# Performance work log

Hardware: AMD Instinct MI355X
Metric: run time of the kernel (lower is better)

Reference implementation:

```python
import jax, jax.numpy as jnp
import numpy as np

# dims: batch, seq, d_model, d_hidden, routed experts, top-k, shared experts
B, S, D, H, E_R, K, E_S = 2, 1024, 1024, 512, 64, 6, 2
EPS = 1.1920929e-07  # torch.finfo(float32).eps, RMSNorm default when eps=None


def setup_inputs() -> dict:
    key = jax.random.key(0)
    ks = jax.random.split(key, 8)
    u = lambda k, shape, b: jax.random.uniform(k, shape, jnp.float32, -b, b)
    bd = 1.0 / np.sqrt(D)   # bound for W1 (1/sqrt(d_input)) and W2 (1/sqrt(d_output)=1/sqrt(D))
    bh = 1.0 / np.sqrt(H)
    return {
        "x": jax.random.normal(ks[0], (B, S, D), jnp.float32),
        "norm_w": jnp.ones((D,), jnp.float32),            # RMSNorm weight
        "Wr": u(ks[1], (E_R, D), bd),                      # router Linear weight (no bias)
        "sW1": u(ks[2], (E_S, D, H), bd), "sb1": jnp.zeros((E_S, 1, H), jnp.float32),
        "sW2": u(ks[3], (E_S, H, D), bd), "sb2": jnp.zeros((E_S, 1, D), jnp.float32),
        "sWg": u(ks[4], (H, H), bh),                       # shared-experts SwiGLU gate weight
        "rW1": u(ks[5], (E_R, D, H), bd), "rb1": jnp.zeros((E_R, 1, H), jnp.float32),
        "rW2": u(ks[6], (E_R, H, D), bd), "rb2": jnp.zeros((E_R, 1, D), jnp.float32),
        "rWg": u(ks[7], (H, H), bh),                       # routed-experts SwiGLU gate weight
        "bias": jnp.full((E_R,), 1.0 / E_R, jnp.float32), # routing bias buffer (expert_bias=True)
    }


def _rmsnorm(x, w):
    ms = jnp.mean(x * x, axis=-1, keepdims=True)
    return x * jax.lax.rsqrt(ms + EPS) * w


def _swiglu(h, Wg):
    # SwiGLU(d_model=H): silu(h @ Wg) * h, elementwise gate over hidden dim
    return jax.nn.silu(h @ Wg) * h


def reference(x, norm_w, Wr, sW1, sb1, sW2, sb2, sWg, rW1, rb1, rW2, rb2, rWg, bias):
    xn = _rmsnorm(x, norm_w)
    t = xn.reshape(-1, D)                                  # (T, D) tokens
    # --- shared experts, summed over expert axis ---
    hs = jnp.einsum('td,edh->teh', t, sW1) + sb1[None, :, 0, :]
    hs = _swiglu(hs, sWg)
    shared = jnp.einsum('teh,ehd->td', hs, sW2) + jnp.sum(sb2[:, 0, :], axis=0)
    # --- router ---
    raw = t @ Wr.T                                         # (T, E_R) raw affinity
    aff = jax.lax.stop_gradient(raw) + bias                # detached + bias for top-k selection
    _, idx = jax.lax.top_k(aff, K)                         # (T, K)
    # --- routed experts: dense all-expert FFN, gather top-k outputs ---
    # (mathematically identical to the source's per-token weight gather,
    #  but avoids materializing (T,K,D,H) weight tensors)
    h = jnp.einsum('td,edh->teh', t, rW1) + rb1[None, :, 0, :]   # (T, E_R, H)
    h = _swiglu(h, rWg)
    out_all = jnp.einsum('teh,ehd->ted', h, rW2) + rb2[None, :, 0, :]  # (T, E_R, D)
    out_k = jnp.take_along_axis(out_all, idx[:, :, None], axis=1)      # (T, K, D)
    aff_k = jnp.take_along_axis(raw, idx, axis=1)                      # (T, K) raw (undetached)
    w = aff_k / jnp.sum(aff_k, axis=-1, keepdims=True)                 # expert_bias=True path
    routed = jnp.einsum('tk,tkd->td', w, out_k)                        # (T, D)
    return x + (shared + routed).reshape(B, S, D)
```

## Files before the change

### kernel.cpp

```cpp
#include <hip/hip_runtime.h>
#include <cstdint>
#include <cstddef>

typedef unsigned short u16;
typedef unsigned int u32;
typedef __attribute__((ext_vector_type(8))) short bh8;
typedef __attribute__((ext_vector_type(4))) float fx4;

#define T_TOK 2048
#define D_DIM 1024
#define H_DIM 512
#define N_EXP 64
#define K_TOP 6
#define N_ASG (T_TOK * K_TOP)

__device__ __forceinline__ float bf2f(u16 v) {
    union { u32 u; float f; } c; c.u = ((u32)v) << 16; return c.f;
}
__device__ __forceinline__ u16 f2bf(float f) {
    union { u32 u; float f; } c; c.f = f;
    u32 u = c.u;
    return (u16)((u + 0x7fffu + ((u >> 16) & 1u)) >> 16);
}

__global__ __launch_bounds__(256) void rmsnorm_k(
    const float* __restrict__ x, const float* __restrict__ nw, u16* __restrict__ xnb)
{
    int t = blockIdx.x, tid = threadIdx.x;
    int d0 = tid << 2;
    float4 xv = *(const float4*)(x + (size_t)t * D_DIM + d0);
    float ss = xv.x * xv.x + xv.y * xv.y + xv.z * xv.z + xv.w * xv.w;
    #pragma unroll
    for (int o = 32; o > 0; o >>= 1) ss += __shfl_down(ss, o);
    __shared__ float red[4];
    if ((tid & 63) == 0) red[tid >> 6] = ss;
    __syncthreads();
    float ms = (red[0] + red[1] + red[2] + red[3]) * (1.f / (float)D_DIM);
    float sc = rsqrtf(ms + 1.1920929e-07f);
    float4 wv = *(const float4*)(nw + d0);
    ushort4 ob;
    ob.x = f2bf(xv.x * sc * wv.x);
    ob.y = f2bf(xv.y * sc * wv.y);
    ob.z = f2bf(xv.z * sc * wv.z);
    ob.w = f2bf(xv.w * sc * wv.w);
    *(ushort4*)(xnb + (size_t)t * D_DIM + d0) = ob;
}

__global__ __launch_bounds__(256) void routernorm_k(
    const float* __restrict__ x, const float* __restrict__ nw,
    const float* __restrict__ Wr, float* __restrict__ raw)
{
    int t = blockIdx.x, tid = threadIdx.x;
    __shared__ float xs[D_DIM];
    __shared__ float ps[256];
    __shared__ float red[4];
    int d0 = tid << 2;
    float4 xv = *(const float4*)(x + (size_t)t * D_DIM + d0);
    float ss = xv.x * xv.x + xv.y * xv.y + xv.z * xv.z + xv.w * xv.w;
    #pragma unroll
    for (int o = 32; o > 0; o >>= 1) ss += __shfl_down(ss, o);
    if ((tid & 63) == 0) red[tid >> 6] = ss;
    __syncthreads();
    float ms = (red[0] + red[1] + red[2] + red[3]) * (1.f / (float)D_DIM);
    float sc = rsqrtf(ms + 1.1920929e-07f);
    float4 wv = *(const float4*)(nw + d0);
    float4 xf;
    xf.x = xv.x * sc * wv.x;
    xf.y = xv.y * sc * wv.y;
    xf.z = xv.z * sc * wv.z;
    xf.w = xv.w * sc * wv.w;
    *(float4*)&xs[d0] = xf;
    __syncthreads();
    int e = tid & 63, part = tid >> 6;
    const float* wr = Wr + (size_t)e * D_DIM + part * 256;
    const float* xp = &xs[part * 256];
    float s = 0.f;
    #pragma unroll 8
    for (int i = 0; i < 256; i += 4) {
        float4 w4 = *(const float4*)(wr + i);
        s += xp[i] * w4.x + xp[i + 1] * w4.y + xp[i + 2] * w4.z + xp[i + 3] * w4.w;
    }
    ps[tid] = s;
    __syncthreads();
    if (part == 0) raw[(size_t)t * N_EXP + e] = ps[e] + ps[64 + e] + ps[128 + e] + ps[192 + e];
}

__global__ void topk_k(const float* __restrict__ raw, const float* __restrict__ ebias,
                       int* __restrict__ cnt, int* __restrict__ tki, float* __restrict__ tkw)
{
    int t = blockIdx.x, lane = threadIdx.x;
    float r = raw[(size_t)t * N_EXP + lane];
    float cur = r + ebias[lane];
    int selI[K_TOP]; float selR[K_TOP];
    #pragma unroll
    for (int k = 0; k < K_TOP; ++k) {
        float v = cur; int id = lane;
        #pragma unroll
        for (int o = 32; o > 0; o >>= 1) {
            float v2 = __shfl_down(v, o); int i2 = __shfl_down(id, o);
            if (v2 > v || (v2 == v && i2 < id)) { v = v2; id = i2; }
        }
        id = __shfl(id, 0);
        if (lane == id) cur = -3.4e38f;
        selI[k] = id;
        selR[k] = __shfl(r, id);
    }
    float s = 0.f;
    #pragma unroll
    for (int k = 0; k < K_TOP; ++k) s += selR[k];
    if (lane < K_TOP) {
        tki[t * K_TOP + lane] = selI[lane];
        tkw[t * K_TOP + lane] = selR[lane] / s;
        atomicAdd(&cnt[selI[lane]], 1);
    }
}

__global__ void scan_k(const int* __restrict__ cnt, int* __restrict__ offs, int* __restrict__ fill)
{
    if (threadIdx.x == 0) {
        int s = 0;
        for (int e = 0; e < N_EXP; ++e) { offs[e] = s; fill[e] = s; s += cnt[e]; }
        offs[N_EXP] = s;
    }
}

__global__ void fill_k(const int* __restrict__ tki, const float* __restrict__ tkw,
                       int* __restrict__ fill, int* __restrict__ atok, float* __restrict__ aw)
{
    int t = blockIdx.x, lane = threadIdx.x;
    if (lane < K_TOP) {
        int e = tki[t * K_TOP + lane];
        int p = atomicAdd(&fill[e], 1);
        atok[p] = t;
        aw[p] = tkw[t * K_TOP + lane];
    }
}

__global__ __launch_bounds__(256) void convF_k(
    const float* __restrict__ in, u16* __restrict__ out, int K, int N)
{
    int mat = blockIdx.z;
    size_t mo = (size_t)mat * K * N;
    int n0 = blockIdx.x << 6, k0 = blockIdx.y << 6;
    __shared__ u16 t[64][72];
    int tid = threadIdx.x;
    int kr = tid >> 4, c4 = (tid & 15) << 2;
    #pragma unroll
    for (int rr = 0; rr < 4; ++rr) {
        int k = (rr << 4) + kr;
        float4 v = *(const float4*)(in + mo + (size_t)(k0 + k) * N + n0 + c4);
        t[c4 + 0][k] = f2bf(v.x);
        t[c4 + 1][k] = f2bf(v.y);
        t[c4 + 2][k] = f2bf(v.z);
        t[c4 + 3][k] = f2bf(v.w);
    }
    __syncthreads();
    int lane = tid & 63, g = tid >> 6;
    int nr = lane & 15, kq = lane >> 4;
    #pragma unroll
    for (int f = 0; f < 2; ++f) {
        int fragId = g + (f << 2);
        int ntile = fragId >> 1, kb = fragId & 1;
        bh8 v = *(const bh8*)&t[(ntile << 4) + nr][(kb << 5) + (kq << 3)];
        size_t fi = (((size_t)((n0 >> 4) + ntile) * (size_t)(K >> 5)
                      + (size_t)((k0 >> 5) + kb)) << 9) + (size_t)(lane << 3);
        *(bh8*)(out + mo + fi) = v;
    }
}

__global__ __launch_bounds__(256) void moe_ffn3_k(
    const u16* __restrict__ xnb,
    const u16* __restrict__ W1f,
    const u16* __restrict__ Wgf,
    const u16* __restrict__ W2f,
    const float* __restrict__ rb1, const float* __restrict__ rb2,
    const float* __restrict__ sb1, const float* __restrict__ sb2,
    const int* __restrict__ offs, const int* __restrict__ atok,
    const float* __restrict__ aw, float* __restrict__ accG)
{
    int e = blockIdx.x;
    bool routed = e < N_EXP;
    int start = routed ? offs[e] : 0;
    int end   = routed ? offs[e + 1] : T_TOK;
    int rowBase = start + (blockIdx.y << 5);
    if (rowBase >= end) return;
    int rows = end - rowBase; if (rows > 32) rows = 32;

    __shared__ int   tok[32];
    __shared__ float wt[32];
    __shared__ u16 hbuf[33280];
    u16* hA = hbuf;
    u16* hG = hbuf + 16640;

    int tid = threadIdx.x;
    if (tid < 32) {
        int cl = rowBase + tid; if (cl >= end) cl = end - 1;
        tok[tid] = routed ? atok[cl] : cl;
        wt[tid]  = routed ? aw[cl] : 1.0f;
    }
    __syncthreads();

    {
        u16* Ast = hbuf;
        #pragma unroll
        for (int p = 0; p < 16; ++p) {
            int r = (p << 1) + (tid >> 7);
            int c = (tid & 127) << 3;
            *(uint4*)&Ast[r * 1032 + c] = *(const uint4*)(xnb + (size_t)tok[r] * D_DIM + c);
        }
    }
    __syncthreads();

    int w = tid >> 6, lane = tid & 63, quad = lane >> 4, l15 = lane & 15;
    int n0w = w << 7;

    const u16* W1e = W1f + (size_t)e * (H_DIM * D_DIM);
    const u16* W2e = W2f + (size_t)e * (H_DIM * D_DIM);
    const u16* Wge = Wgf + (routed ? 0 : (size_t)(H_DIM * H_DIM));
    const float* b1 = routed ? rb1 + e * H_DIM : sb1 + (e - N_EXP) * H_DIM;
    const float* b2 = routed ? rb2 + e * D_DIM : sb2 + (e - N_EXP) * D_DIM;

    {
        const u16* Ast = hbuf;
        const u16* bp = W1e + ((size_t)w << 17) + (lane << 3);
        fx4 ac0[8] = {}, ac1[8] = {};
        #pragma unroll 2
        for (int kbi = 0; kbi < 32; ++kbi) {
            bh8 a0 = *(const bh8*)&Ast[l15 * 1032 + (kbi << 5) + (quad << 3)];
            bh8 a1 = *(const bh8*)&Ast[(16 + l15) * 1032 + (kbi << 5) + (quad << 3)];
            #pragma unroll
            for (int ct = 0; ct < 8; ++ct) {
                bh8 b = *(const bh8*)(bp + (((ct << 5) + kbi) << 9));
                ac0[ct] = __builtin_amdgcn_mfma_f32_16x16x32_bf16(a0, b, ac0[ct], 0, 0, 0);
                ac1[ct] = __builtin_amdgcn_mfma_f32_16x16x32_bf16(a1, b, ac1[ct], 0, 0, 0);
            }
        }
        __syncthreads();
        #pragma unroll
        for (int ct = 0; ct < 8; ++ct) {
            int col = n0w + (ct << 4) + l15;
            float bv = b1[col];
            #pragma unroll
            for (int r = 0; r < 4; ++r) {
                int r0 = (quad << 2) + r;
                hA[r0 * 520 + col]        = f2bf(ac0[ct][r] + bv);
                hA[(16 + r0) * 520 + col] = f2bf(ac1[ct][r] + bv);
            }
        }
    }
    __syncthreads();

    {
        const u16* bp = Wge + ((size_t)w << 16) + (lane << 3);
        fx4 ac0[8] = {}, ac1[8] = {};
        #pragma unroll 2
        for (int kbi = 0; kbi < 16; ++kbi) {
            bh8 a0 = *(const bh8*)&hA[l15 * 520 + (kbi << 5) + (quad << 3)];
            bh8 a1 = *(const bh8*)&hA[(16 + l15) * 520 + (kbi << 5) + (quad << 3)];
            #pragma unroll
            for (int ct = 0; ct < 8; ++ct) {
                bh8 b = *(const bh8*)(bp + (((ct << 4) + kbi) << 9));
                ac0[ct] = __builtin_amdgcn_mfma_f32_16x16x32_bf16(a0, b, ac0[ct], 0, 0, 0);
                ac1[ct] = __builtin_amdgcn_mfma_f32_16x16x32_bf16(a1, b, ac1[ct], 0, 0, 0);
            }
        }
        #pragma unroll
        for (int ct = 0; ct < 8; ++ct) {
            int col = n0w + (ct << 4) + l15;
            #pragma unroll
            for (int r = 0; r < 4; ++r) {
                int r0 = (quad << 2) + r;
                float g0 = ac0[ct][r];
                float h0 = bf2f(hA[r0 * 520 + col]);
                hG[r0 * 520 + col] = f2bf(h0 * g0 * (1.f / (1.f + __expf(-g0))));
                int r1 = 16 + r0;
                float g1 = ac1[ct][r];
                float h1 = bf2f(hA[r1 * 520 + col]);
                hG[r1 * 520 + col] = f2bf(h1 * g1 * (1.f / (1.f + __expf(-g1))));
            }
        }
    }
    __syncthreads();

    #pragma unroll 1
    for (int half = 0; half < 2; ++half) {
        int n0 = (w << 8) + (half << 7);
        const u16* bp = W2e + (((size_t)((w << 4) + (half << 3))) << 13) + (lane << 3);
        fx4 ac0[8] = {}, ac1[8] = {};
        #pragma unroll 2
        for (int kbi = 0; kbi < 16; ++kbi) {
            bh8 a0 = *(const bh8*)&hG[l15 * 520 + (kbi << 5) + (quad << 3)];
            bh8 a1 = *(const bh8*)&hG[(16 + l15) * 520 + (kbi << 5) + (quad << 3)];
            #pragma unroll
            for (int ct = 0; ct < 8; ++ct) {
                bh8 b = *(const bh8*)(bp + (((ct << 4) + kbi) << 9));
                ac0[ct] = __builtin_amdgcn_mfma_f32_16x16x32_bf16(a0, b, ac0[ct], 0, 0, 0);
                ac1[ct] = __builtin_amdgcn_mfma_f32_16x16x32_bf16(a1, b, ac1[ct], 0, 0, 0);
            }
        }
        #pragma unroll
        for (int ct = 0; ct < 8; ++ct) {
            int col = n0 + (ct << 4) + l15;
            float bv = b2[col];
            #pragma unroll
            for (int r = 0; r < 4; ++r) {
                int r0 = (quad << 2) + r;
                if (r0 < rows)
                    atomicAdd(&accG[(size_t)tok[r0] * D_DIM + col], wt[r0] * (ac0[ct][r] + bv));
                int r1 = 16 + r0;
                if (r1 < rows)
                    atomicAdd(&accG[(size_t)tok[r1] * D_DIM + col], wt[r1] * (ac1[ct][r] + bv));
            }
        }
    }
}

template<int ROUTED>
__global__ __launch_bounds__(256) void moe_ffn_k(
    const u16* __restrict__ xnb,
    const float* __restrict__ W1b, const float* __restrict__ Wg,
    const float* __restrict__ W2b,
    const float* __restrict__ b1b, const float* __restrict__ b2b,
    const int* __restrict__ offs, const int* __restrict__ atok,
    const float* __restrict__ aw, float* __restrict__ accG)
{
    int e = blockIdx.z;
    int start = ROUTED ? offs[e] : 0;
    int end   = ROUTED ? offs[e + 1] : T_TOK;
    int rowBase = start + (blockIdx.y << 5);
    if (rowBase >= end) return;
    int rows = end - rowBase; if (rows > 32) rows = 32;

    __shared__ int   tok[32];
    __shared__ float wt[32];
    __shared__ u16 hA[32 * 520];
    __shared__ u16 hG[32 * 520];
    __shared__ u16 As[32 * 32];
    __shared__ u16 Bs[64 * 36];

    int tid = threadIdx.x;
    if (tid < 32) {
        int cl = rowBase + tid; if (cl >= end) cl = end - 1;
        tok[tid] = ROUTED ? atok[cl] : cl;
        wt[tid]  = ROUTED ? aw[cl] : 1.0f;
    }
    __syncthreads();

    const float* W1 = W1b + (size_t)e * (D_DIM * H_DIM);
    const float* W2 = W2b + (size_t)e * (D_DIM * H_DIM);
    const float* b1 = b1b + e * H_DIM;
    const float* b2 = b2b + e * D_DIM;

    int w = tid >> 6, lane = tid & 63, quad = lane >> 4, l15 = lane & 15;
    int sr2 = tid >> 3, sc2 = (tid & 7) << 2;

    for (int nc = 0; nc < 8; ++nc) {
        int n0 = nc << 6;
        fx4 a0 = {}; fx4 a1 = {};
        for (int kc = 0; kc < 32; ++kc) {
            int kb = kc << 5;
            int2 av = *(const int2*)(xnb + (size_t)tok[sr2] * D_DIM + kb + sc2);
            const float* cp = W1 + n0 + lane;
            int kx = kb + (w << 3);
            u32 p[4];
            #pragma unroll
            for (int jj = 0; jj < 4; ++jj) {
                u32 lo = f2bf(cp[(size_t)(kx + 2 * jj) * H_DIM]);
                u32 hi = f2bf(cp[(size_t)(kx + 2 * jj + 1) * H_DIM]);
                p[jj] = lo | (hi << 16);
            }
            __syncthreads();
            *(int2*)&As[sr2 * 32 + sc2] = av;
            u16* bsw = &Bs[lane * 36 + (w << 3)];
            uint2 q0; q0.x = p[0]; q0.y = p[1];
            uint2 q1; q1.x = p[2]; q1.y = p[3];
            *(uint2*)bsw = q0;
            *(uint2*)(bsw + 4) = q1;
            __syncthreads();
            bh8 af0 = *(const bh8*)&As[l15 * 32 + (quad << 3)];
            bh8 af1 = *(const bh8*)&As[(16 + l15) * 32 + (quad << 3)];
            const u16* brp = &Bs[((w << 4) + l15) * 36 + (quad << 3)];
            union { bh8 v; uint2 u2[2]; } bf;
            bf.u2[0] = *(const uint2*)brp;
            bf.u2[1] = *(const uint2*)(brp + 4);
            a0 = __builtin_amdgcn_mfma_f32_16x16x32_bf16(af0, bf.v, a0, 0, 0, 0);
            a1 = __builtin_amdgcn_mfma_f32_16x16x32_bf16(af1, bf.v, a1, 0, 0, 0);
        }
        int col = n0 + (w << 4) + l15;
        float bv = b1[col];
        #pragma unroll
        for (int r = 0; r < 4; ++r) {
            hA[((quad << 2) + r) * 520 + col]      = f2bf(a0[r] + bv);
            hA[(16 + (quad << 2) + r) * 520 + col] = f2bf(a1[r] + bv);
        }
    }
    __syncthreads();

    for (int nc = 0; nc < 8; ++nc) {
        int n0 = nc << 6;
        fx4 a0 = {}; fx4 a1 = {};
        for (int kc = 0; kc < 16; ++kc) {
            int kb = kc << 5;
            const float* cp = Wg + n0 + lane;
            int kx = kb + (w << 3);
            u32 p[4];
            #pragma unroll
            for (int jj = 0; jj < 4; ++jj) {
                u32 lo = f2bf(cp[(size_t)(kx + 2 * jj) * H_DIM]);
                u32 hi = f2bf(cp[(size_t)(kx + 2 * jj + 1) * H_DIM]);
                p[jj] = lo | (hi << 16);
            }
            __syncthreads();
            u16* bsw = &Bs[lane * 36 + (w << 3)];
            uint2 q0; q0.x = p[0]; q0.y = p[1];
            uint2 q1; q1.x = p[2]; q1.y = p[3];
            *(uint2*)bsw = q0;
            *(uint2*)(bsw + 4) = q1;
            __syncthreads();
            bh8 af0 = *(const bh8*)&hA[l15 * 520 + kb + (quad << 3)];
            bh8 af1 = *(const bh8*)&hA[(16 + l15) * 520 + kb + (quad << 3)];
            const u16* brp = &Bs[((w << 4) + l15) * 36 + (quad << 3)];
            union { bh8 v; uint2 u2[2]; } bf;
            bf.u2[0] = *(const uint2*)brp;
            bf.u2[1] = *(const uint2*)(brp + 4);
            a0 = __builtin_amdgcn_mfma_f32_16x16x32_bf16(af0, bf.v, a0, 0, 0, 0);
            a1 = __builtin_amdgcn_mfma_f32_16x16x32_bf16(af1, bf.v, a1, 0, 0, 0);
        }
        int col = n0 + (w << 4) + l15;
        #pragma unroll
        for (int r = 0; r < 4; ++r) {
            int r0 = (quad << 2) + r;
            float h0 = bf2f(hA[r0 * 520 + col]);
            float g0 = a0[r];
            hG[r0 * 520 + col] = f2bf(h0 * g0 * (1.f / (1.f + __expf(-g0))));
            int r1 = 16 + r0;
            float h1 = bf2f(hA[r1 * 520 + col]);
            float g1 = a1[r];
            hG[r1 * 520 + col] = f2bf(h1 * g1 * (1.f / (1.f + __expf(-g1))));
        }
    }
    __syncthreads();

    for (int nc = 0; nc < 16; ++nc) {
        int n0 = nc << 6;
        fx4 a0 = {}; fx4 a1 = {};
        for (int kc = 0; kc < 16; ++kc) {
            int kb = kc << 5;
            const float* cp = W2 + n0 + lane;
            int kx = kb + (w << 3);
            u32 p[4];
            #pragma unroll
            for (int jj = 0; jj < 4; ++jj) {
                u32 lo = f2bf(cp[(size_t)(kx + 2 * jj) * D_DIM]);
                u32 hi = f2bf(cp[(size_t)(kx + 2 * jj + 1) * D_DIM]);
                p[jj] = lo | (hi << 16);
            }
            __syncthreads();
            u16* bsw = &Bs[lane * 36 + (w << 3)];
            uint2 q0; q0.x = p[0]; q0.y = p[1];
            uint2 q1; q1.x = p[2]; q1.y = p[3];
            *(uint2*)bsw = q0;
            *(uint2*)(bsw + 4) = q1;
            __syncthreads();
            bh8 af0 = *(const bh8*)&hG[l15 * 520 + kb + (quad << 3)];
            bh8 af1 = *(const bh8*)&hG[(16 + l15) * 520 + kb + (quad << 3)];
            const u16* brp = &Bs[((w << 4) + l15) * 36 + (quad << 3)];
            union { bh8 v; uint2 u2[2]; } bf;
            bf.u2[0] = *(const uint2*)brp;
            bf.u2[1] = *(const uint2*)(brp + 4);
            a0 = __builtin_amdgcn_mfma_f32_16x16x32_bf16(af0, bf.v, a0, 0, 0, 0);
            a1 = __builtin_amdgcn_mfma_f32_16x16x32_bf16(af1, bf.v, a1, 0, 0, 0);
        }
        int col = n0 + (w << 4) + l15;
        float bv = b2[col];
        #pragma unroll
        for (int r = 0; r < 4; ++r) {
            int lr0 = (quad << 2) + r;
            if (lr0 < rows)
                atomicAdd(&accG[(size_t)tok[lr0] * D_DIM + col], wt[lr0] * (a0[r] + bv));
            int lr1 = 16 + lr0;
            if (lr1 < rows)
                atomicAdd(&accG[(size_t)tok[lr1] * D_DIM + col], wt[lr1] * (a1[r] + bv));
        }
    }
}

__global__ __launch_bounds__(256) void final_k(
    const float* __restrict__ x, const float* __restrict__ acc, float* __restrict__ out)
{
    size_t i = ((size_t)blockIdx.x * 256 + threadIdx.x) << 2;
    float4 xv = *(const float4*)(x + i);
    float4 a = *(const float4*)(acc + i);
    float4 o;
    o.x = xv.x + a.x;
    o.y = xv.y + a.y;
    o.z = xv.z + a.z;
    o.w = xv.w + a.w;
    *(float4*)(out + i) = o;
}

extern "C" void kernel_launch(void* const* d_in, const int* in_sizes, int n_in,
                              void* d_out, int out_size, void* d_ws, size_t ws_size,
                              hipStream_t stream)
{
    const float* x     = (const float*)d_in[0];
    const float* nw    = (const float*)d_in[1];
    const float* Wr    = (const float*)d_in[2];
    const float* sW1   = (const float*)d_in[3];
    const float* sb1   = (const float*)d_in[4];
    const float* sW2   = (const float*)d_in[5];
    const float* sb2   = (const float*)d_in[6];
    const float* sWg   = (const float*)d_in[7];
    const float* rW1   = (const float*)d_in[8];
    const float* rb1   = (const float*)d_in[9];
    const float* rW2   = (const float*)d_in[10];
    const float* rb2   = (const float*)d_in[11];
    const float* rWg   = (const float*)d_in[12];
    const float* ebias = (const float*)d_in[13];
    float* out = (float*)d_out;
    (void)in_sizes; (void)n_in; (void)out_size;

    char* wp = (char*)d_ws;
    auto alloc = [&](size_t b) { char* p = wp; wp += (b + 255) & ~(size_t)255; return p; };
    int*   cnt  = (int*)alloc(N_EXP * 4);
    int*   offs = (int*)alloc((N_EXP + 1) * 4);
    int*   fill = (int*)alloc(N_EXP * 4);
    int*   tki  = (int*)alloc((size_t)T_TOK * K_TOP * 4);
    float* tkw  = (float*)alloc((size_t)T_TOK * K_TOP * 4);
    int*   atok = (int*)alloc((size_t)N_ASG * 4);
    float* aw   = (float*)alloc((size_t)N_ASG * 4);
    float* raw  = (float*)alloc((size_t)T_TOK * N_EXP * 4);
    u16*   xnb  = (u16*)alloc((size_t)T_TOK * D_DIM * 2);
    float* acc  = (float*)alloc((size_t)T_TOK * D_DIM * 4);
    u16* W1f = (u16*)alloc((size_t)(N_EXP + 2) * H_DIM * D_DIM * 2);
    u16* W2f = (u16*)alloc((size_t)(N_EXP + 2) * H_DIM * D_DIM * 2);
    u16* Wgf = (u16*)alloc((size_t)2 * H_DIM * H_DIM * 2);
    bool fast = (size_t)(wp - (char*)d_ws) <= ws_size;

    hipMemsetAsync(cnt, 0, N_EXP * 4, stream);
    hipMemsetAsync(acc, 0, (size_t)T_TOK * D_DIM * 4, stream);

    dim3 b256(256);
    rmsnorm_k<<<T_TOK, b256, 0, stream>>>(x, nw, xnb);
    routernorm_k<<<T_TOK, b256, 0, stream>>>(x, nw, Wr, raw);
    topk_k<<<T_TOK, dim3(64), 0, stream>>>(raw, ebias, cnt, tki, tkw);
    scan_k<<<1, dim3(64), 0, stream>>>(cnt, offs, fill);
    fill_k<<<T_TOK, dim3(64), 0, stream>>>(tki, tkw, fill, atok, aw);

    if (fast) {
        size_t ms = (size_t)H_DIM * D_DIM;
        convF_k<<<dim3(H_DIM / 64, D_DIM / 64, N_EXP), b256, 0, stream>>>(rW1, W1f, D_DIM, H_DIM);
        convF_k<<<dim3(H_DIM / 64, D_DIM / 64, 2), b256, 0, stream>>>(sW1, W1f + (size_t)N_EXP * ms, D_DIM, H_DIM);
        convF_k<<<dim3(D_DIM / 64, H_DIM / 64, N_EXP), b256, 0, stream>>>(rW2, W2f, H_DIM, D_DIM);
        convF_k<<<dim3(D_DIM / 64, H_DIM / 64, 2), b256, 0, stream>>>(sW2, W2f + (size_t)N_EXP * ms, H_DIM, D_DIM);
        convF_k<<<dim3(H_DIM / 64, H_DIM / 64, 1), b256, 0, stream>>>(rWg, Wgf, H_DIM, H_DIM);
        convF_k<<<dim3(H_DIM / 64, H_DIM / 64, 1), b256, 0, stream>>>(sWg, Wgf + (size_t)H_DIM * H_DIM, H_DIM, H_DIM);

        moe_ffn3_k<<<dim3(N_EXP + 2, 64, 1), b256, 0, stream>>>(
            xnb, W1f, Wgf, W2f, rb1, rb2, sb1, sb2, offs, atok, aw, acc);
    } else {
        moe_ffn_k<1><<<dim3(1, 64, N_EXP), b256, 0, stream>>>(
            xnb, rW1, rWg, rW2, rb1, rb2, offs, atok, aw, acc);
        moe_ffn_k<0><<<dim3(1, 64, 2), b256, 0, stream>>>(
            xnb, sW1, sWg, sW2, sb1, sb2, offs, atok, aw, acc);
    }

    final_k<<<(T_TOK * D_DIM) / 1024, b256, 0, stream>>>(x, acc, out);
}
```

Before: 741.1 us.

## Fuse RMSNorm into router, stream A from global, double-buffer MFMA loads, XCD-aware grid

Drops the separate rmsnorm kernel by writing the bf16 normalized activations from the router-norm kernel. The MoE FFN kernel no longer stages the token rows in LDS. It reads A fragments directly from global and software-pipelines the A/B register loads across k-steps with a two-stage double buffer. It reuses a single hidden buffer in LDS, which cuts shared memory per block and may raise occupancy. The grid is flattened and remapped so that each expert's row slabs land on one XCD, aiming for better L2 reuse of weights, at the cost of uncached global gathers for A and more register pressure.

```diff
diff --git a/kernel.cpp b/kernel.cpp
--- a/kernel.cpp
+++ b/kernel.cpp
@@ -23,32 +23,9 @@
     return (u16)((u + 0x7fffu + ((u >> 16) & 1u)) >> 16);
 }
 
-__global__ __launch_bounds__(256) void rmsnorm_k(
-    const float* __restrict__ x, const float* __restrict__ nw, u16* __restrict__ xnb)
-{
-    int t = blockIdx.x, tid = threadIdx.x;
-    int d0 = tid << 2;
-    float4 xv = *(const float4*)(x + (size_t)t * D_DIM + d0);
-    float ss = xv.x * xv.x + xv.y * xv.y + xv.z * xv.z + xv.w * xv.w;
-    #pragma unroll
-    for (int o = 32; o > 0; o >>= 1) ss += __shfl_down(ss, o);
-    __shared__ float red[4];
-    if ((tid & 63) == 0) red[tid >> 6] = ss;
-    __syncthreads();
-    float ms = (red[0] + red[1] + red[2] + red[3]) * (1.f / (float)D_DIM);
-    float sc = rsqrtf(ms + 1.1920929e-07f);
-    float4 wv = *(const float4*)(nw + d0);
-    ushort4 ob;
-    ob.x = f2bf(xv.x * sc * wv.x);
-    ob.y = f2bf(xv.y * sc * wv.y);
-    ob.z = f2bf(xv.z * sc * wv.z);
-    ob.w = f2bf(xv.w * sc * wv.w);
-    *(ushort4*)(xnb + (size_t)t * D_DIM + d0) = ob;
-}
-
 __global__ __launch_bounds__(256) void routernorm_k(
     const float* __restrict__ x, const float* __restrict__ nw,
-    const float* __restrict__ Wr, float* __restrict__ raw)
+    const float* __restrict__ Wr, float* __restrict__ raw, u16* __restrict__ xnb)
 {
     int t = blockIdx.x, tid = threadIdx.x;
     __shared__ float xs[D_DIM];
@@ -70,6 +47,9 @@
     xf.z = xv.z * sc * wv.z;
     xf.w = xv.w * sc * wv.w;
     *(float4*)&xs[d0] = xf;
+    ushort4 ob;
+    ob.x = f2bf(xf.x); ob.y = f2bf(xf.y); ob.z = f2bf(xf.z); ob.w = f2bf(xf.w);
+    *(ushort4*)(xnb + (size_t)t * D_DIM + d0) = ob;
     __syncthreads();
     int e = tid & 63, part = tid >> 6;
     const float* wr = Wr + (size_t)e * D_DIM + part * 256;
@@ -168,7 +148,7 @@
     }
 }
 
-__global__ __launch_bounds__(256) void moe_ffn3_k(
+__global__ __launch_bounds__(256) void moe_ffn4_k(
     const u16* __restrict__ xnb,
     const u16* __restrict__ W1f,
     const u16* __restrict__ Wgf,
@@ -178,19 +158,29 @@
     const int* __restrict__ offs, const int* __restrict__ atok,
     const float* __restrict__ aw, float* __restrict__ accG)
 {
-    int e = blockIdx.x;
-    bool routed = e < N_EXP;
-    int start = routed ? offs[e] : 0;
-    int end   = routed ? offs[e + 1] : T_TOK;
-    int rowBase = start + (blockIdx.y << 5);
+    int id = blockIdx.x;
+    int xcd = id & 7, rest = id >> 3, grp = rest >> 6, slab = rest & 63;
+    int e, rowBase, end;
+    bool routed;
+    if (grp < 8) {
+        e = (grp << 3) + xcd;
+        routed = true;
+        rowBase = offs[e] + (slab << 5);
+        end = offs[e + 1];
+    } else {
+        int f = (slab << 3) + xcd;
+        if (f >= 128) return;
+        e = N_EXP + (f & 1);
+        routed = false;
+        rowBase = (f >> 1) << 5;
+        end = T_TOK;
+    }
     if (rowBase >= end) return;
     int rows = end - rowBase; if (rows > 32) rows = 32;
 
     __shared__ int   tok[32];
     __shared__ float wt[32];
-    __shared__ u16 hbuf[33280];
-    u16* hA = hbuf;
-    u16* hG = hbuf + 16640;
+    __shared__ u16 hA[32 * 520];
 
     int tid = threadIdx.x;
     if (tid < 32) {
@@ -200,17 +190,6 @@
     }
     __syncthreads();
 
-    {
-        u16* Ast = hbuf;
-        #pragma unroll
-        for (int p = 0; p < 16; ++p) {
-            int r = (p << 1) + (tid >> 7);
-            int c = (tid & 127) << 3;
-            *(uint4*)&Ast[r * 1032 + c] = *(const uint4*)(xnb + (size_t)tok[r] * D_DIM + c);
-        }
-    }
-    __syncthreads();
-
     int w = tid >> 6, lane = tid & 63, quad = lane >> 4, l15 = lane & 15;
     int n0w = w << 7;
 
@@ -221,21 +200,36 @@
     const float* b2 = routed ? rb2 + e * D_DIM : sb2 + (e - N_EXP) * D_DIM;
 
     {
-        const u16* Ast = hbuf;
-        const u16* bp = W1e + ((size_t)w << 17) + (lane << 3);
+        const u16* a0p = xnb + (size_t)tok[l15] * D_DIM + (quad << 3);
+        const u16* a1p = xnb + (size_t)tok[16 + l15] * D_DIM + (quad << 3);
+        const u16* bp  = W1e + ((size_t)w << 17) + (lane << 3);
         fx4 ac0[8] = {}, ac1[8] = {};
-        #pragma unroll 2
-        for (int kbi = 0; kbi < 32; ++kbi) {
-            bh8 a0 = *(const bh8*)&Ast[l15 * 1032 + (kbi << 5) + (quad << 3)];
-            bh8 a1 = *(const bh8*)&Ast[(16 + l15) * 1032 + (kbi << 5) + (quad << 3)];
+        bh8 bA[8], bB[8], aA0, aA1, aB0, aB1;
+        #pragma unroll
+        for (int ct = 0; ct < 8; ++ct) bA[ct] = *(const bh8*)(bp + (ct << 14));
+        aA0 = *(const bh8*)a0p;
+        aA1 = *(const bh8*)a1p;
+        #pragma unroll 1
+        for (int kbi = 0; kbi < 32; kbi += 2) {
+            #pragma unroll
+            for (int ct = 0; ct < 8; ++ct) bB[ct] = *(const bh8*)(bp + (((ct << 5) + kbi + 1) << 9));
+            aB0 = *(const bh8*)(a0p + ((kbi + 1) << 5));
+            aB1 = *(const bh8*)(a1p + ((kbi + 1) << 5));
             #pragma unroll
             for (int ct = 0; ct < 8; ++ct) {
-                bh8 b = *(const bh8*)(bp + (((ct << 5) + kbi) << 9));
-                ac0[ct] = __builtin_amdgcn_mfma_f32_16x16x32_bf16(a0, b, ac0[ct], 0, 0, 0);
-                ac1[ct] = __builtin_amdgcn_mfma_f32_16x16x32_bf16(a1, b, ac1[ct], 0, 0, 0);
-            }
-        }
-        __syncthreads();
+                ac0[ct] = __builtin_amdgcn_mfma_f32_16x16x32_bf16(aA0, bA[ct], ac0[ct], 0, 0, 0);
+                ac1[ct] = __builtin_amdgcn_mfma_f32_16x16x32_bf16(aA1, bA[ct], ac1[ct], 0, 0, 0);
+            }
+            #pragma unroll
+            for (int ct = 0; ct < 8; ++ct) bA[ct] = *(const bh8*)(bp + (((ct << 5) + kbi + 2) << 9));
+            aA0 = *(const bh8*)(a0p + ((kbi + 2) << 5));
+            aA1 = *(const bh8*)(a1p + ((kbi + 2) << 5));
+            #pragma unroll
+            for (int ct = 0; ct < 8; ++ct) {
+                ac0[ct] = __builtin_amdgcn_mfma_f32_16x16x32_bf16(aB0, bB[ct], ac0[ct], 0, 0, 0);
+                ac1[ct] = __builtin_amdgcn_mfma_f32_16x16x32_bf16(aB1, bB[ct], ac1[ct], 0, 0, 0);
+            }
+        }
         #pragma unroll
         for (int ct = 0; ct < 8; ++ct) {
             int col = n0w + (ct << 4) + l15;
@@ -251,19 +245,37 @@
     __syncthreads();
 
     {
+        const u16* A0 = hA + l15 * 520 + (quad << 3);
+        const u16* A1 = hA + (16 + l15) * 520 + (quad << 3);
         const u16* bp = Wge + ((size_t)w << 16) + (lane << 3);
         fx4 ac0[8] = {}, ac1[8] = {};
-        #pragma unroll 2
-        for (int kbi = 0; kbi < 16; ++kbi) {
-            bh8 a0 = *(const bh8*)&hA[l15 * 520 + (kbi << 5) + (quad << 3)];
-            bh8 a1 = *(const bh8*)&hA[(16 + l15) * 520 + (kbi << 5) + (quad << 3)];
+        bh8 bA[8], bB[8], aA0, aA1, aB0, aB1;
+        #pragma unroll
+        for (int ct = 0; ct < 8; ++ct) bA[ct] = *(const bh8*)(bp + (ct << 13));
+        aA0 = *(const bh8*)A0;
+        aA1 = *(const bh8*)A1;
+        #pragma unroll 1
+        for (int kbi = 0; kbi < 16; kbi += 2) {
+            #pragma unroll
+            for (int ct = 0; ct < 8; ++ct) bB[ct] = *(const bh8*)(bp + (((ct << 4) + kbi + 1) << 9));
+            aB0 = *(const bh8*)(A0 + ((kbi + 1) << 5));
+            aB1 = *(const bh8*)(A1 + ((kbi + 1) << 5));
             #pragma unroll
             for (int ct = 0; ct < 8; ++ct) {
-                bh8 b = *(const bh8*)(bp + (((ct << 4) + kbi) << 9));
-                ac0[ct] = __builtin_amdgcn_mfma_f32_16x16x32_bf16(a0, b, ac0[ct], 0, 0, 0);
-                ac1[ct] = __builtin_amdgcn_mfma_f32_16x16x32_bf16(a1, b, ac1[ct], 0, 0, 0);
-            }
-        }
+                ac0[ct] = __builtin_amdgcn_mfma_f32_16x16x32_bf16(aA0, bA[ct], ac0[ct], 0, 0, 0);
+                ac1[ct] = __builtin_amdgcn_mfma_f32_16x16x32_bf16(aA1, bA[ct], ac1[ct], 0, 0, 0);
+            }
+            #pragma unroll
+            for (int ct = 0; ct < 8; ++ct) bA[ct] = *(const bh8*)(bp + (((ct << 4) + kbi + 2) << 9));
+            aA0 = *(const bh8*)(A0 + ((kbi + 2) << 5));
+            aA1 = *(const bh8*)(A1 + ((kbi + 2) << 5));
+            #pragma unroll
+            for (int ct = 0; ct < 8; ++ct) {
+                ac0[ct] = __builtin_amdgcn_mfma_f32_16x16x32_bf16(aB0, bB[ct], ac0[ct], 0, 0, 0);
+                ac1[ct] = __builtin_amdgcn_mfma_f32_16x16x32_bf16(aB1, bB[ct], ac1[ct], 0, 0, 0);
+            }
+        }
+        __syncthreads();
         #pragma unroll
         for (int ct = 0; ct < 8; ++ct) {
             int col = n0w + (ct << 4) + l15;
@@ -272,11 +284,11 @@
                 int r0 = (quad << 2) + r;
                 float g0 = ac0[ct][r];
                 float h0 = bf2f(hA[r0 * 520 + col]);
-                hG[r0 * 520 + col] = f2bf(h0 * g0 * (1.f / (1.f + __expf(-g0))));
+                hA[r0 * 520 + col] = f2bf(h0 * g0 * (1.f / (1.f + __expf(-g0))));
                 int r1 = 16 + r0;
                 float g1 = ac1[ct][r];
                 float h1 = bf2f(hA[r1 * 520 + col]);
-                hG[r1 * 520 + col] = f2bf(h1 * g1 * (1.f / (1.f + __expf(-g1))));
+                hA[r1 * 520 + col] = f2bf(h1 * g1 * (1.f / (1.f + __expf(-g1))));
             }
         }
     }
@@ -285,17 +297,34 @@
     #pragma unroll 1
     for (int half = 0; half < 2; ++half) {
         int n0 = (w << 8) + (half << 7);
+        const u16* A0 = hA + l15 * 520 + (quad << 3);
+        const u16* A1 = hA + (16 + l15) * 520 + (quad << 3);
         const u16* bp = W2e + (((size_t)((w << 4) + (half << 3))) << 13) + (lane << 3);
         fx4 ac0[8] = {}, ac1[8] = {};
-        #pragma unroll 2
-        for (int kbi = 0; kbi < 16; ++kbi) {
-            bh8 a0 = *(const bh8*)&hG[l15 * 520 + (kbi << 5) + (quad << 3)];
-            bh8 a1 = *(const bh8*)&hG[(16 + l15) * 520 + (kbi << 5) + (quad << 3)];
+        bh8 bA[8], bB[8], aA0, aA1, aB0, aB1;
+        #pragma unroll
+        for (int ct = 0; ct < 8; ++ct) bA[ct] = *(const bh8*)(bp + (ct << 13));
+        aA0 = *(const bh8*)A0;
+        aA1 = *(const bh8*)A1;
+        #pragma unroll 1
+        for (int kbi = 0; kbi < 16; kbi += 2) {
+            #pragma unroll
+            for (int ct = 0; ct < 8; ++ct) bB[ct] = *(const bh8*)(bp + (((ct << 4) + kbi + 1) << 9));
+            aB0 = *(const bh8*)(A0 + ((kbi + 1) << 5));
+            aB1 = *(const bh8*)(A1 + ((kbi + 1) << 5));
             #pragma unroll
             for (int ct = 0; ct < 8; ++ct) {
-                bh8 b = *(const bh8*)(bp + (((ct << 4) + kbi) << 9));
-                ac0[ct] = __builtin_amdgcn_mfma_f32_16x16x32_bf16(a0, b, ac0[ct], 0, 0, 0);
-                ac1[ct] = __builtin_amdgcn_mfma_f32_16x16x32_bf16(a1, b, ac1[ct], 0, 0, 0);
+                ac0[ct] = __builtin_amdgcn_mfma_f32_16x16x32_bf16(aA0, bA[ct], ac0[ct], 0, 0, 0);
+                ac1[ct] = __builtin_amdgcn_mfma_f32_16x16x32_bf16(aA1, bA[ct], ac1[ct], 0, 0, 0);
+            }
+            #pragma unroll
+            for (int ct = 0; ct < 8; ++ct) bA[ct] = *(const bh8*)(bp + (((ct << 4) + kbi + 2) << 9));
+            aA0 = *(const bh8*)(A0 + ((kbi + 2) << 5));
+            aA1 = *(const bh8*)(A1 + ((kbi + 2) << 5));
+            #pragma unroll
+            for (int ct = 0; ct < 8; ++ct) {
+                ac0[ct] = __builtin_amdgcn_mfma_f32_16x16x32_bf16(aB0, bB[ct], ac0[ct], 0, 0, 0);
+                ac1[ct] = __builtin_amdgcn_mfma_f32_16x16x32_bf16(aB1, bB[ct], ac1[ct], 0, 0, 0);
             }
         }
         #pragma unroll
@@ -535,14 +564,14 @@
     u16* W1f = (u16*)alloc((size_t)(N_EXP + 2) * H_DIM * D_DIM * 2);
     u16* W2f = (u16*)alloc((size_t)(N_EXP + 2) * H_DIM * D_DIM * 2);
     u16* Wgf = (u16*)alloc((size_t)2 * H_DIM * H_DIM * 2);
+    alloc(1 << 16);
     bool fast = (size_t)(wp - (char*)d_ws) <= ws_size;
 
     hipMemsetAsync(cnt, 0, N_EXP * 4, stream);
     hipMemsetAsync(acc, 0, (size_t)T_TOK * D_DIM * 4, stream);
 
     dim3 b256(256);
-    rmsnorm_k<<<T_TOK, b256, 0, stream>>>(x, nw, xnb);
-    routernorm_k<<<T_TOK, b256, 0, stream>>>(x, nw, Wr, raw);
+    routernorm_k<<<T_TOK, b256, 0, stream>>>(x, nw, Wr, raw, xnb);
     topk_k<<<T_TOK, dim3(64), 0, stream>>>(raw, ebias, cnt, tki, tkw);
     scan_k<<<1, dim3(64), 0, stream>>>(cnt, offs, fill);
     fill_k<<<T_TOK, dim3(64), 0, stream>>>(tki, tkw, fill, atok, aw);
@@ -556,7 +585,7 @@
         convF_k<<<dim3(H_DIM / 64, H_DIM / 64, 1), b256, 0, stream>>>(rWg, Wgf, H_DIM, H_DIM);
         convF_k<<<dim3(H_DIM / 64, H_DIM / 64, 1), b256, 0, stream>>>(sWg, Wgf + (size_t)H_DIM * H_DIM, H_DIM, H_DIM);
 
-        moe_ffn3_k<<<dim3(N_EXP + 2, 64, 1), b256, 0, stream>>>(
+        moe_ffn4_k<<<dim3(8 * 9 * 64), b256, 0, stream>>>(
             xnb, W1f, Wgf, W2f, rb1, rb2, sb1, sb2, offs, atok, aw, acc);
     } else {
         moe_ffn_k<1><<<dim3(1, 64, N_EXP), b256, 0, stream>>>(
```

Result: no change. 755.7 us (+2.0%).
